# Kernel tuning notes

Measured on AMD Instinct MI355X. Metric: run time of the kernel, lower is better.

The kernel has to match this reference:

```python
import jax, jax.numpy as jnp
import numpy as np

D_MODEL = 1024
NUM_HEADS = 16
D_HEAD = D_MODEL // NUM_HEADS
ROPE_BASE = 10000.0


def _rope(x):
    # x: (B, H, S, Dh); lucidrains interleaved rotary along seq dim
    dh = x.shape[-1]
    s = x.shape[-2]
    inv_freq = 1.0 / (ROPE_BASE ** (jnp.arange(0, dh, 2, dtype=jnp.float32) / dh))
    freqs = jnp.arange(s, dtype=jnp.float32)[:, None] * inv_freq[None, :]  # (S, Dh/2)
    cos = jnp.repeat(jnp.cos(freqs), 2, axis=-1)  # (S, Dh), [f0,f0,f1,f1,...]
    sin = jnp.repeat(jnp.sin(freqs), 2, axis=-1)
    x1 = x[..., ::2]
    x2 = x[..., 1::2]
    rot = jnp.stack([-x2, x1], axis=-1).reshape(x.shape)  # rotate_half, interleaved
    return x * cos + rot * sin


def setup_inputs() -> dict:
    key = jax.random.key(0)
    ks = jax.random.split(key, 16)
    B, S, D, H, Dh = 8, 1024, D_MODEL, NUM_HEADS, D_HEAD
    scale = 1.0 / np.sqrt(D)
    inp = {
        "query": jax.random.normal(ks[0], (B, S, D), jnp.float32),
        "key": jax.random.normal(ks[1], (B, S, D), jnp.float32),
        "value": jax.random.normal(ks[2], (B, S, D), jnp.float32),
        "mask": jax.random.randint(ks[3], (B, S, S), 0, 2).astype(bool),
        "Wq": jax.random.normal(ks[4], (D, D), jnp.float32) * scale,
        "bq": jnp.zeros((D,), jnp.float32),
        "Wk": jax.random.normal(ks[5], (D, D), jnp.float32) * scale,
        "bk": jnp.zeros((D,), jnp.float32),
        "Wv": jax.random.normal(ks[6], (D, D), jnp.float32) * scale,
        "bv": jnp.zeros((D,), jnp.float32),
        "u_bias": jax.random.normal(ks[7], (H, Dh), jnp.float32) * (1.0 / np.sqrt(Dh)),
        "Wo": jax.random.normal(ks[8], (D, D), jnp.float32) * scale,
        "bo": jnp.zeros((D,), jnp.float32),
    }
    return inp


def reference(query, key, value, mask, Wq, bq, Wk, bk, Wv, bv, u_bias, Wo, bo):
    B, S, D = query.shape
    H, Dh = NUM_HEADS, D_HEAD
    # projections -> (B, H, S, Dh)
    q = (query @ Wq.T + bq).reshape(B, S, H, Dh).transpose(0, 2, 1, 3)
    k = (key @ Wk.T + bk).reshape(B, S, H, Dh).transpose(0, 2, 1, 3)
    v = (value @ Wv.T + bv).reshape(B, S, H, Dh).transpose(0, 2, 1, 3)
    q = _rope(q)  # (B, H, S, Dh)
    k = _rope(k)
    # (q + u_bias) @ k^T ; u_bias broadcasts over (H, Dh)
    qb = q + u_bias[None, :, None, :]
    score = jnp.einsum("bhsd,bhtd->bhst", qb, k) / np.sqrt(Dh)
    score = jnp.where(mask[:, None, :, :], -1e9, score)
    attn = jax.nn.softmax(score, axis=-1)  # dropout is identity in eval mode
    ctx = jnp.einsum("bhst,bhtd->bhsd", attn, v)  # (B, H, S, Dh)
    ctx = ctx.transpose(0, 2, 1, 3).reshape(B, S, D)
    return ctx @ Wo.T + bo
```

## Files before the change

kernel.cpp:

```cpp
#include <hip/hip_runtime.h>

#define S_LEN 1024
#define D_MODELX 1024
#define NHEAD 16
#define DHEAD 64
#define BATCH 8
#define NTOK (BATCH * S_LEN)
#define KSCALE 0.18033688011112f

typedef __bf16 bf16;
typedef __attribute__((ext_vector_type(8))) __bf16 bf16x8;
typedef __attribute__((ext_vector_type(4))) __bf16 bf16x4;
typedef __attribute__((ext_vector_type(4))) float f32x4;

__device__ __forceinline__ void gload_lds16(const void* gsrc, void* ldst) {
  __builtin_amdgcn_global_load_lds(
      (const __attribute__((address_space(1))) void*)gsrc,
      (__attribute__((address_space(3))) void*)ldst,
      16, 0, 0);
}

#define PRE_ACT_BLKS 8192
#define PRE_W_BLKS 1024
#define PRE_MASK_BLKS 32768
#define PRE_TOTAL (3 * PRE_ACT_BLKS + 4 * PRE_W_BLKS + PRE_MASK_BLKS + 128)
__global__ __launch_bounds__(256) void preproc(
    const float* __restrict__ q, const float* __restrict__ k,
    const float* __restrict__ v, const float* __restrict__ Wq,
    const float* __restrict__ Wk, const float* __restrict__ Wv,
    const float* __restrict__ Wo, const int* __restrict__ mask,
    bf16* __restrict__ Xq, bf16* __restrict__ Xk, bf16* __restrict__ Xv,
    bf16* __restrict__ Wqb, bf16* __restrict__ Wkb, bf16* __restrict__ Wvb,
    bf16* __restrict__ Wob, unsigned long long* __restrict__ mp,
    float* __restrict__ cosT, float* __restrict__ sinT) {
  int blk = blockIdx.x;
  int tid = threadIdx.x;
  if (blk < 3 * PRE_ACT_BLKS + 4 * PRE_W_BLKS) {
    const float* src;
    bf16* dst;
    int l;
    if (blk < PRE_ACT_BLKS) { src = q; dst = Xq; l = blk; }
    else if (blk < 2 * PRE_ACT_BLKS) { src = k; dst = Xk; l = blk - PRE_ACT_BLKS; }
    else if (blk < 3 * PRE_ACT_BLKS) { src = v; dst = Xv; l = blk - 2 * PRE_ACT_BLKS; }
    else if (blk < 3 * PRE_ACT_BLKS + PRE_W_BLKS) { src = Wq; dst = Wqb; l = blk - 3 * PRE_ACT_BLKS; }
    else if (blk < 3 * PRE_ACT_BLKS + 2 * PRE_W_BLKS) { src = Wk; dst = Wkb; l = blk - 3 * PRE_ACT_BLKS - PRE_W_BLKS; }
    else if (blk < 3 * PRE_ACT_BLKS + 3 * PRE_W_BLKS) { src = Wv; dst = Wvb; l = blk - 3 * PRE_ACT_BLKS - 2 * PRE_W_BLKS; }
    else { src = Wo; dst = Wob; l = blk - 3 * PRE_ACT_BLKS - 3 * PRE_W_BLKS; }
    int i = l * 256 + tid;
    float4 val = ((const float4*)src)[i];
    bf16x4 o;
    o[0] = (bf16)val.x; o[1] = (bf16)val.y; o[2] = (bf16)val.z; o[3] = (bf16)val.w;
    ((bf16x4*)dst)[i] = o;
  } else if (blk < 3 * PRE_ACT_BLKS + 4 * PRE_W_BLKS + PRE_MASK_BLKS) {
    int l = blk - (3 * PRE_ACT_BLKS + 4 * PRE_W_BLKS);
    int i = l * 256 + tid;
    unsigned long long bal = __ballot(mask[i] != 0);
    if ((tid & 63) == 0) mp[i >> 6] = bal;
  } else {
    int l = blk - (3 * PRE_ACT_BLKS + 4 * PRE_W_BLKS + PRE_MASK_BLKS);
    int idx = l * 256 + tid;
    int s = idx >> 5;
    int i = idx & 31;
    float inv = powf(10000.0f, -(float)i / 32.0f);
    float f = (float)s * inv;
    cosT[idx] = cosf(f);
    sinT[idx] = sinf(f);
  }
}

__global__ __launch_bounds__(256) void gemm_qkv(
    const bf16* __restrict__ Xq, const bf16* __restrict__ Xk,
    const bf16* __restrict__ Xv, const bf16* __restrict__ W3,
    const float* __restrict__ bq, const float* __restrict__ bk,
    const float* __restrict__ bv,
    bf16* __restrict__ qws, bf16* __restrict__ kws, bf16* __restrict__ vws,
    const float* __restrict__ cosT, const float* __restrict__ sinT,
    const float* __restrict__ ubias) {
  __shared__ bf16 At[128 * 64];
  __shared__ bf16 Bt[128 * 64];
  const int id = blockIdx.x;
  const int xcd = id & 7;
  const int idx = id >> 3;
  const int mpan = xcd * 8 + idx / 24;
  const int nblk = idx % 24;
  const int m0 = mpan * 128;
  const int n0 = nblk * 128;
  const int proj = nblk >> 3;
  const bf16* X = proj == 0 ? Xq : proj == 1 ? Xk : Xv;
  const float* bias = proj == 0 ? bq : proj == 1 ? bk : bv;

  const int tid = threadIdx.x;
  const int lane = tid & 63;
  const int wid = tid >> 6;
  const int g = lane >> 4;
  const int li = lane & 15;
  const int wr = (wid >> 1) * 64;
  const int wc = (wid & 1) * 64;

  f32x4 acc[4][4] = {};

  for (int k0 = 0; k0 < D_MODELX; k0 += 64) {
    __syncthreads();
#pragma unroll
    for (int c = 0; c < 4; ++c) {
      int chunk = (c * 4 + wid) * 64 + lane;
      int r = chunk >> 3;
      int seg = (chunk & 7) ^ (r & 7);
      gload_lds16(X + (size_t)(m0 + r) * D_MODELX + k0 + seg * 8,
                  &At[((c * 4 + wid) * 64) * 8]);
      gload_lds16(W3 + (size_t)(n0 + r) * D_MODELX + k0 + seg * 8,
                  &Bt[((c * 4 + wid) * 64) * 8]);
    }
    __syncthreads();
#pragma unroll
    for (int kk = 0; kk < 2; ++kk) {
      bf16x8 af[4], bfr[4];
#pragma unroll
      for (int m = 0; m < 4; ++m) {
        int row = wr + m * 16 + li;
        af[m] = *(const bf16x8*)&At[row * 64 + (((kk * 4 + g) ^ (row & 7)) << 3)];
      }
#pragma unroll
      for (int n = 0; n < 4; ++n) {
        int row = wc + n * 16 + li;
        bfr[n] = *(const bf16x8*)&Bt[row * 64 + (((kk * 4 + g) ^ (row & 7)) << 3)];
      }
#pragma unroll
      for (int m = 0; m < 4; ++m)
#pragma unroll
        for (int n = 0; n < 4; ++n)
          acc[m][n] = __builtin_amdgcn_mfma_f32_16x16x32_bf16(af[m], bfr[n],
                                                              acc[m][n], 0, 0, 0);
    }
  }

#pragma unroll
  for (int m = 0; m < 4; ++m) {
#pragma unroll
    for (int n = 0; n < 4; ++n) {
      int col = n0 + wc + n * 16 + li;
      int col1k = col & 1023;
      int dh = col1k & 63;
      int h = col1k >> 6;
      if (proj == 2) {
        int token0 = m0 + wr + m * 16 + g * 4;
        int s0 = token0 & (S_LEN - 1);
        int b0 = token0 >> 10;
        bf16x4 o;
#pragma unroll
        for (int rg = 0; rg < 4; ++rg) o[rg] = (bf16)(acc[m][n][rg] + bias[col1k]);
        *(bf16x4*)&vws[(((size_t)b0 * NHEAD + h) * DHEAD + dh) * S_LEN + s0] = o;
      } else {
#pragma unroll
        for (int rg = 0; rg < 4; ++rg) {
          int token = m0 + wr + m * 16 + g * 4 + rg;
          float v = acc[m][n][rg] + bias[col1k];
          float p = __shfl_xor(v, 1, 64);
          int s = token & (S_LEN - 1);
          int b = token >> 10;
          int fi = dh >> 1;
          float cv = cosT[s * 32 + fi];
          float sv = sinT[s * 32 + fi];
          float vr = (dh & 1) ? (v * cv + p * sv) : (v * cv - p * sv);
          if (proj == 0) {
            vr += ubias[(h << 6) + dh];
            qws[(((size_t)b * NHEAD + h) * S_LEN + s) * DHEAD + dh] = (bf16)vr;
          } else {
            kws[(((size_t)b * NHEAD + h) * S_LEN + s) * DHEAD + dh] = (bf16)(vr * KSCALE);
          }
        }
      }
    }
  }
}

__global__ __launch_bounds__(256) void gemm_out(
    const bf16* __restrict__ X, const bf16* __restrict__ W,
    const float* __restrict__ bias, float* __restrict__ outp) {
  __shared__ bf16 At[128 * 64];
  __shared__ bf16 Bt[128 * 64];
  const int id = blockIdx.x;
  const int swz = (id & 7) * 64 + (id >> 3);
  const int m0 = (swz >> 3) * 128;
  const int n0 = (swz & 7) * 128;
  const int tid = threadIdx.x;
  const int lane = tid & 63;
  const int wid = tid >> 6;
  const int g = lane >> 4;
  const int li = lane & 15;
  const int wr = (wid >> 1) * 64;
  const int wc = (wid & 1) * 64;

  f32x4 acc[4][4] = {};

  for (int k0 = 0; k0 < D_MODELX; k0 += 64) {
    __syncthreads();
#pragma unroll
    for (int c = 0; c < 4; ++c) {
      int chunk = (c * 4 + wid) * 64 + lane;
      int r = chunk >> 3;
      int seg = (chunk & 7) ^ (r & 7);
      gload_lds16(X + (size_t)(m0 + r) * D_MODELX + k0 + seg * 8,
                  &At[((c * 4 + wid) * 64) * 8]);
      gload_lds16(W + (size_t)(n0 + r) * D_MODELX + k0 + seg * 8,
                  &Bt[((c * 4 + wid) * 64) * 8]);
    }
    __syncthreads();
#pragma unroll
    for (int kk = 0; kk < 2; ++kk) {
      bf16x8 af[4], bfr[4];
#pragma unroll
      for (int m = 0; m < 4; ++m) {
        int row = wr + m * 16 + li;
        af[m] = *(const bf16x8*)&At[row * 64 + (((kk * 4 + g) ^ (row & 7)) << 3)];
      }
#pragma unroll
      for (int n = 0; n < 4; ++n) {
        int row = wc + n * 16 + li;
        bfr[n] = *(const bf16x8*)&Bt[row * 64 + (((kk * 4 + g) ^ (row & 7)) << 3)];
      }
#pragma unroll
      for (int m = 0; m < 4; ++m)
#pragma unroll
        for (int n = 0; n < 4; ++n)
          acc[m][n] = __builtin_amdgcn_mfma_f32_16x16x32_bf16(af[m], bfr[n],
                                                              acc[m][n], 0, 0, 0);
    }
  }

#pragma unroll
  for (int m = 0; m < 4; ++m)
#pragma unroll
    for (int n = 0; n < 4; ++n) {
      int col = n0 + wc + n * 16 + li;
#pragma unroll
      for (int rg = 0; rg < 4; ++rg) {
        int token = m0 + wr + m * 16 + g * 4 + rg;
        outp[(size_t)token * D_MODELX + col] = acc[m][n][rg] + bias[col];
      }
    }
}

__global__ __launch_bounds__(256) void attn_fwd(
    const bf16* __restrict__ Q, const bf16* __restrict__ K,
    const bf16* __restrict__ V, const unsigned long long* __restrict__ mp,
    bf16* __restrict__ ctx) {
  __shared__ bf16 Kl[2][64 * 64];
  __shared__ bf16 Vt[2][64 * 64];
  __shared__ bf16 Pl[4][16 * 64];

  const int id = blockIdx.x;
  const int swz = (id & 7) * 256 + (id >> 3);
  const int bh = swz >> 4;
  const int qblk = swz & 15;
  const int tid = threadIdx.x;
  const int lane = tid & 63;
  const int wid = tid >> 6;
  const int b = bh >> 4;
  const int h = bh & 15;
  const int g = lane >> 4;
  const int li = lane & 15;
  const int q0 = qblk * 64 + wid * 16;

  const bf16* qbase = Q + ((size_t)bh * S_LEN + q0) * DHEAD;
  bf16x8 qf[2];
  qf[0] = *(const bf16x8*)&qbase[(size_t)li * DHEAD + g * 8];
  qf[1] = *(const bf16x8*)&qbase[(size_t)li * DHEAD + 32 + g * 8];

  bf16x8 onesf;
#pragma unroll
  for (int j = 0; j < 8; ++j) onesf[j] = (bf16)1.0f;

  f32x4 ctxacc[4] = {};
  f32x4 sacc = {};

  const bf16* gk = K + (size_t)bh * S_LEN * DHEAD;
  const bf16* gv = V + (size_t)bh * DHEAD * S_LEN;
  const unsigned long long* mrowp = mp + ((size_t)b * S_LEN + q0) * 16;

  const int srow = lane >> 3;
  const int schunk = (lane & 7) ^ srow;

  auto stage = [&](int bi, int it) {
    int t0 = it * 64;
#pragma unroll
    for (int j = 0; j < 2; ++j) {
      int row = wid * 16 + j * 8 + srow;
      gload_lds16(gk + ((size_t)(t0 + row)) * DHEAD + schunk * 8,
                  &Kl[bi][(wid * 16 + j * 8) * 64]);
      gload_lds16(gv + (size_t)row * S_LEN + t0 + schunk * 8,
                  &Vt[bi][(wid * 16 + j * 8) * 64]);
    }
  };

  stage(0, 0);
  int buf = 0;

  for (int it = 0; it < S_LEN / 64; ++it) {
    asm volatile("s_waitcnt vmcnt(0)" ::: "memory");
    __builtin_amdgcn_s_barrier();
    if (it + 1 < S_LEN / 64) stage(buf ^ 1, it + 1);

    unsigned long long mw[4];
#pragma unroll
    for (int rg = 0; rg < 4; ++rg)
      mw[rg] = mrowp[(size_t)(g * 4 + rg) * 16 + it];

    f32x4 sc[4];
    __builtin_amdgcn_s_setprio(1);
#pragma unroll
    for (int tt = 0; tt < 4; ++tt) {
      int row = tt * 16 + li;
      int sz = li & 7;
      bf16x8 kf0 = *(const bf16x8*)&Kl[buf][row * 64 + ((g ^ sz) << 3)];
      bf16x8 kf1 = *(const bf16x8*)&Kl[buf][row * 64 + (((g + 4) ^ sz) << 3)];
      f32x4 a = {};
      a = __builtin_amdgcn_mfma_f32_16x16x32_bf16(qf[0], kf0, a, 0, 0, 0);
      a = __builtin_amdgcn_mfma_f32_16x16x32_bf16(qf[1], kf1, a, 0, 0, 0);
      sc[tt] = a;
    }
    __builtin_amdgcn_s_setprio(0);

#pragma unroll
    for (int rg = 0; rg < 4; ++rg) {
      unsigned long long msh = mw[rg] >> li;
      unsigned int mlo = (unsigned int)msh;
      unsigned int mhi = (unsigned int)(msh >> 32);
      int qq = g * 4 + rg;
#pragma unroll
      for (int tt = 0; tt < 4; ++tt) {
        unsigned int half = (tt & 2) ? mhi : mlo;
        unsigned int bit = (half >> ((tt & 1) << 4)) & 1u;
        float p = exp2f(sc[tt][rg]);
        p = bit ? 0.0f : p;
        int t = tt * 16 + li;
        Pl[wid][qq * 64 + (t ^ ((qq & 7) << 3))] = (bf16)p;
      }
    }

    __builtin_amdgcn_s_setprio(1);
#pragma unroll
    for (int sub = 0; sub < 2; ++sub) {
      bf16x8 pf = *(const bf16x8*)&Pl[wid][li * 64 + (((sub * 4 + g) ^ (li & 7)) << 3)];
      sacc = __builtin_amdgcn_mfma_f32_16x16x32_bf16(pf, onesf, sacc, 0, 0, 0);
#pragma unroll
      for (int dd = 0; dd < 4; ++dd) {
        int row = dd * 16 + li;
        bf16x8 vf = *(const bf16x8*)&Vt[buf][row * 64 + (((sub * 4 + g) ^ (row & 7)) << 3)];
        ctxacc[dd] = __builtin_amdgcn_mfma_f32_16x16x32_bf16(pf, vf, ctxacc[dd], 0, 0, 0);
      }
    }
    __builtin_amdgcn_s_setprio(0);
    buf ^= 1;
  }

  float inv[4];
#pragma unroll
  for (int rg = 0; rg < 4; ++rg) inv[rg] = 1.0f / sacc[rg];
#pragma unroll
  for (int dd = 0; dd < 4; ++dd)
#pragma unroll
    for (int rg = 0; rg < 4; ++rg) {
      float vout = ctxacc[dd][rg] * inv[rg];
      int s = q0 + g * 4 + rg;
      int d = h * 64 + dd * 16 + li;
      ctx[((size_t)b * S_LEN + s) * D_MODELX + d] = (bf16)vout;
    }
}

extern "C" void kernel_launch(void* const* d_in, const int* in_sizes, int n_in,
                              void* d_out, int out_size, void* d_ws, size_t ws_size,
                              hipStream_t stream) {
  const float* query = (const float*)d_in[0];
  const float* key   = (const float*)d_in[1];
  const float* value = (const float*)d_in[2];
  const int*   mask  = (const int*)d_in[3];
  const float* Wq = (const float*)d_in[4];
  const float* bq = (const float*)d_in[5];
  const float* Wk = (const float*)d_in[6];
  const float* bk = (const float*)d_in[7];
  const float* Wv = (const float*)d_in[8];
  const float* bv = (const float*)d_in[9];
  const float* ub = (const float*)d_in[10];
  const float* Wo = (const float*)d_in[11];
  const float* bo = (const float*)d_in[12];
  float* out = (float*)d_out;

  char* wsb = (char*)d_ws;
  size_t off = 0;
  auto give = [&](size_t bytes) -> char* {
    char* p = wsb + off;
    off += (bytes + 255) & ~(size_t)255;
    return p;
  };
  const size_t ACT = (size_t)NTOK * D_MODELX * 2;
  const size_t WB  = (size_t)D_MODELX * D_MODELX * 2;
  bf16* Xq   = (bf16*)give(ACT);
  bf16* Xk   = (bf16*)give(ACT);
  bf16* Xv   = (bf16*)give(ACT);
  bf16* Wqb  = (bf16*)give(WB);
  bf16* Wkb  = (bf16*)give(WB);
  bf16* Wvb  = (bf16*)give(WB);
  bf16* Wob  = (bf16*)give(WB);
  bf16* qws  = (bf16*)give(ACT);
  bf16* kws  = (bf16*)give(ACT);
  bf16* vws  = (bf16*)give(ACT);
  unsigned long long* mp = (unsigned long long*)give((size_t)BATCH * S_LEN * 16 * 8);
  float* cosT = (float*)give((size_t)S_LEN * 32 * 4);
  float* sinT = (float*)give((size_t)S_LEN * 32 * 4);
  bf16* ctxw = Xq;

  preproc<<<PRE_TOTAL, 256, 0, stream>>>(query, key, value, Wq, Wk, Wv, Wo, mask,
                                         Xq, Xk, Xv, Wqb, Wkb, Wvb, Wob, mp,
                                         cosT, sinT);

  gemm_qkv<<<1536, 256, 0, stream>>>(Xq, Xk, Xv, Wqb, bq, bk, bv,
                                     qws, kws, vws, cosT, sinT, ub);

  attn_fwd<<<2048, 256, 0, stream>>>(qws, kws, vws, mp, ctxw);

  gemm_out<<<512, 256, 0, stream>>>(ctxw, Wob, bo, out);
}
```

Baseline: 398.9 us.

## Double-buffer LDS tiles in QKV and output GEMMs with async prefetch

Both projection GEMMs now use two LDS buffers and issue the global-to-LDS loads two k-steps ahead. Explicit vmcnt waits and raw barriers replace the two syncthreads per iteration, so memory latency can overlap with MFMA work. The QKV kernel also reorders block-to-tile mapping so that consecutive blocks on an XCD share the same weight panel. LDS use doubles to 64KB per block, which may lower occupancy.

```diff
diff --git a/kernel.cpp b/kernel.cpp
--- a/kernel.cpp
+++ b/kernel.cpp
@@ -76,13 +76,13 @@
     bf16* __restrict__ qws, bf16* __restrict__ kws, bf16* __restrict__ vws,
     const float* __restrict__ cosT, const float* __restrict__ sinT,
     const float* __restrict__ ubias) {
-  __shared__ bf16 At[128 * 64];
-  __shared__ bf16 Bt[128 * 64];
+  __shared__ bf16 At[2][128 * 64];
+  __shared__ bf16 Bt[2][128 * 64];
   const int id = blockIdx.x;
   const int xcd = id & 7;
   const int idx = id >> 3;
-  const int mpan = xcd * 8 + idx / 24;
-  const int nblk = idx % 24;
+  const int nblk = idx >> 3;
+  const int mpan = xcd * 8 + (idx & 7);
   const int m0 = mpan * 128;
   const int n0 = nblk * 128;
   const int proj = nblk >> 3;
@@ -99,31 +99,43 @@
 
   f32x4 acc[4][4] = {};
 
-  for (int k0 = 0; k0 < D_MODELX; k0 += 64) {
-    __syncthreads();
+  auto stage = [&](int bi, int k0) {
 #pragma unroll
     for (int c = 0; c < 4; ++c) {
       int chunk = (c * 4 + wid) * 64 + lane;
       int r = chunk >> 3;
       int seg = (chunk & 7) ^ (r & 7);
       gload_lds16(X + (size_t)(m0 + r) * D_MODELX + k0 + seg * 8,
-                  &At[((c * 4 + wid) * 64) * 8]);
+                  &At[bi][((c * 4 + wid) * 64) * 8]);
       gload_lds16(W3 + (size_t)(n0 + r) * D_MODELX + k0 + seg * 8,
-                  &Bt[((c * 4 + wid) * 64) * 8]);
-    }
-    __syncthreads();
+                  &Bt[bi][((c * 4 + wid) * 64) * 8]);
+    }
+  };
+
+  stage(0, 0);
+  stage(1, 64);
+
+  const int NT = D_MODELX / 64;
+  for (int t = 0; t < NT; ++t) {
+    if (t < NT - 1)
+      asm volatile("s_waitcnt vmcnt(8)" ::: "memory");
+    else
+      asm volatile("s_waitcnt vmcnt(0)" ::: "memory");
+    __builtin_amdgcn_s_barrier();
+    const int bi = t & 1;
+    __builtin_amdgcn_s_setprio(1);
 #pragma unroll
     for (int kk = 0; kk < 2; ++kk) {
       bf16x8 af[4], bfr[4];
 #pragma unroll
       for (int m = 0; m < 4; ++m) {
         int row = wr + m * 16 + li;
-        af[m] = *(const bf16x8*)&At[row * 64 + (((kk * 4 + g) ^ (row & 7)) << 3)];
+        af[m] = *(const bf16x8*)&At[bi][row * 64 + (((kk * 4 + g) ^ (row & 7)) << 3)];
       }
 #pragma unroll
       for (int n = 0; n < 4; ++n) {
         int row = wc + n * 16 + li;
-        bfr[n] = *(const bf16x8*)&Bt[row * 64 + (((kk * 4 + g) ^ (row & 7)) << 3)];
+        bfr[n] = *(const bf16x8*)&Bt[bi][row * 64 + (((kk * 4 + g) ^ (row & 7)) << 3)];
       }
 #pragma unroll
       for (int m = 0; m < 4; ++m)
@@ -132,6 +144,10 @@
           acc[m][n] = __builtin_amdgcn_mfma_f32_16x16x32_bf16(af[m], bfr[n],
                                                               acc[m][n], 0, 0, 0);
     }
+    __builtin_amdgcn_s_setprio(0);
+    __builtin_amdgcn_sched_barrier(0);
+    __builtin_amdgcn_s_barrier();
+    if (t + 2 < NT) stage(bi, (t + 2) * 64);
   }
 
 #pragma unroll
@@ -177,8 +193,8 @@
 __global__ __launch_bounds__(256) void gemm_out(
     const bf16* __restrict__ X, const bf16* __restrict__ W,
     const float* __restrict__ bias, float* __restrict__ outp) {
-  __shared__ bf16 At[128 * 64];
-  __shared__ bf16 Bt[128 * 64];
+  __shared__ bf16 At[2][128 * 64];
+  __shared__ bf16 Bt[2][128 * 64];
   const int id = blockIdx.x;
   const int swz = (id & 7) * 64 + (id >> 3);
   const int m0 = (swz >> 3) * 128;
@@ -193,31 +209,43 @@
 
   f32x4 acc[4][4] = {};
 
-  for (int k0 = 0; k0 < D_MODELX; k0 += 64) {
-    __syncthreads();
+  auto stage = [&](int bi, int k0) {
 #pragma unroll
     for (int c = 0; c < 4; ++c) {
       int chunk = (c * 4 + wid) * 64 + lane;
       int r = chunk >> 3;
       int seg = (chunk & 7) ^ (r & 7);
       gload_lds16(X + (size_t)(m0 + r) * D_MODELX + k0 + seg * 8,
-                  &At[((c * 4 + wid) * 64) * 8]);
+                  &At[bi][((c * 4 + wid) * 64) * 8]);
       gload_lds16(W + (size_t)(n0 + r) * D_MODELX + k0 + seg * 8,
-                  &Bt[((c * 4 + wid) * 64) * 8]);
-    }
-    __syncthreads();
+                  &Bt[bi][((c * 4 + wid) * 64) * 8]);
+    }
+  };
+
+  stage(0, 0);
+  stage(1, 64);
+
+  const int NT = D_MODELX / 64;
+  for (int t = 0; t < NT; ++t) {
+    if (t < NT - 1)
+      asm volatile("s_waitcnt vmcnt(8)" ::: "memory");
+    else
+      asm volatile("s_waitcnt vmcnt(0)" ::: "memory");
+    __builtin_amdgcn_s_barrier();
+    const int bi = t & 1;
+    __builtin_amdgcn_s_setprio(1);
 #pragma unroll
     for (int kk = 0; kk < 2; ++kk) {
       bf16x8 af[4], bfr[4];
 #pragma unroll
       for (int m = 0; m < 4; ++m) {
         int row = wr + m * 16 + li;
-        af[m] = *(const bf16x8*)&At[row * 64 + (((kk * 4 + g) ^ (row & 7)) << 3)];
+        af[m] = *(const bf16x8*)&At[bi][row * 64 + (((kk * 4 + g) ^ (row & 7)) << 3)];
       }
 #pragma unroll
       for (int n = 0; n < 4; ++n) {
         int row = wc + n * 16 + li;
-        bfr[n] = *(const bf16x8*)&Bt[row * 64 + (((kk * 4 + g) ^ (row & 7)) << 3)];
+        bfr[n] = *(const bf16x8*)&Bt[bi][row * 64 + (((kk * 4 + g) ^ (row & 7)) << 3)];
       }
 #pragma unroll
       for (int m = 0; m < 4; ++m)
@@ -226,6 +254,10 @@
           acc[m][n] = __builtin_amdgcn_mfma_f32_16x16x32_bf16(af[m], bfr[n],
                                                               acc[m][n], 0, 0, 0);
     }
+    __builtin_amdgcn_s_setprio(0);
+    __builtin_amdgcn_sched_barrier(0);
+    __builtin_amdgcn_s_barrier();
+    if (t + 2 < NT) stage(bi, (t + 2) * 64);
   }
 
 #pragma unroll
```

Result: faster. 382.2 us (-4.2%).
